# Kernel optimization log

Measured on AMD Instinct MI355X. Metric: run time of the kernel, lower is better.

Reference implementation:

```python
import jax, jax.numpy as jnp
import numpy as np


def setup_inputs() -> dict:
    key = jax.random.key(0)
    kq, kk, kv, km = jax.random.split(key, 4)
    B, H, S, D = 8, 16, 1024, 64
    Q = jax.random.normal(kq, (B, H, S, D), dtype=jnp.float32)
    K = jax.random.normal(kk, (B, H, S, D), dtype=jnp.float32)
    V = jax.random.normal(kv, (B, H, S, D), dtype=jnp.float32)
    # True means masked, per torch masked_fill_ semantics
    attn_mask = jax.random.randint(km, (B, 1, S, S), 0, 2).astype(bool)
    return {"Q": Q, "K": K, "V": V, "attn_mask": attn_mask}


def reference(Q, K, V, attn_mask):
    # Attention(Q,K,V) = softmax(QK^T / sqrt(d_k)) V, with masked scores
    # set to 1e-9 (faithful to the original's masked_fill_(mask, 1e-09)).
    d_k = Q.shape[-1]
    scores = jnp.einsum('bhqd,bhkd->bhqk', Q, K) / jnp.sqrt(jnp.float32(d_k))
    scores = jnp.where(attn_mask, jnp.asarray(1e-9, scores.dtype), scores)
    attn = jax.nn.softmax(scores, axis=-1)          # [B,H,S,S]
    context = jnp.einsum('bhqk,bhkd->bhqd', attn, V)  # [B,H,S,D]
    return (context, attn)
```

## Files before the change

kernel.cpp:

```cpp
#include <hip/hip_runtime.h>
#include <hip/hip_bf16.h>

typedef __attribute__((ext_vector_type(4))) float f32x4;
typedef __attribute__((ext_vector_type(8))) short bf16x8;
typedef __attribute__((ext_vector_type(4))) int   i32x4;
typedef __attribute__((ext_vector_type(4))) unsigned u32x4;

#define S_LEN 1024
#define DQ    64
#define QTL   16
#define VSTR  266
#define PSTR  264
#define CSTR  68
#define PT_BYTES (QTL * PSTR * 2)
#define VT_BYTES (DQ * VSTR * 2)

__device__ __forceinline__ unsigned pk2(float a, float b) {
    union { __hip_bfloat162 h; unsigned u; } v;
    v.h = __float22bfloat162_rn(make_float2(a, b));
    return v.u;
}

__device__ __forceinline__ bf16x8 pack8(float4 a, float4 b) {
    union { bf16x8 v; unsigned u[4]; } r;
    r.u[0] = pk2(a.x, a.y); r.u[1] = pk2(a.z, a.w);
    r.u[2] = pk2(b.x, b.y); r.u[3] = pk2(b.z, b.w);
    return r.v;
}

__device__ __forceinline__ bf16x8 ld_frag2(const unsigned short* p) {
    union { bf16x8 v; unsigned u[4]; } r;
    r.u[0] = *(const unsigned*)(p);
    r.u[1] = *(const unsigned*)(p + 2);
    r.u[2] = *(const unsigned*)(p + 16);
    r.u[3] = *(const unsigned*)(p + 18);
    return r.v;
}

__device__ __forceinline__ float bflo(unsigned u) { union { unsigned x; float f; } v; v.x = u << 16;         return v.f; }
__device__ __forceinline__ float bfhi(unsigned u) { union { unsigned x; float f; } v; v.x = u & 0xffff0000u; return v.f; }

__global__ __launch_bounds__(256) void pack_mask(const int* __restrict__ Mg,
                                                 unsigned long long* __restrict__ Pk) {
    const int gw   = (int)((blockIdx.x * 256 + threadIdx.x) >> 6);
    const int lane = threadIdx.x & 63;
#pragma unroll 4
    for (int j = 0; j < 32; ++j) {
        const size_t g = ((size_t)gw * 32 + j) * 64 + lane;
        const int m = __builtin_nontemporal_load(Mg + g);
        const unsigned long long bal = __ballot(m != 0);
        if (lane == 0) Pk[(size_t)gw * 32 + j] = bal;
    }
}

template <int PACKED>
__global__ __launch_bounds__(512, 6) void attn_fused(
    const float* __restrict__ Qg, const float* __restrict__ Kg,
    const float* __restrict__ Vg, const int* __restrict__ Mg,
    const unsigned* __restrict__ Mb,
    float* __restrict__ Og, float* __restrict__ Ag)
{
    const int tid  = threadIdx.x;
    const int lane = tid & 63;
    const int wc   = tid >> 6;
    const int l15  = lane & 15;
    const int lg   = lane >> 4;

    const int raw  = blockIdx.x;
    const int xcd  = raw & 7;
    const int slot = raw >> 3;
    const int bh   = xcd * 16 + (slot >> 6);
    const int qt   = slot & 63;
    const int b    = bh >> 4;

    const size_t kvbase = (size_t)bh * (S_LEN * DQ);
    const float* Qp = Qg + kvbase + (size_t)qt * (QTL * DQ);
    const float* Kp = Kg + kvbase;
    const float* Vp = Vg + kvbase;
    float*       Ap = Ag + (size_t)bh * (size_t)(S_LEN * S_LEN) + (size_t)(qt * QTL) * S_LEN;
    float*       Op = Og + kvbase + (size_t)qt * (QTL * DQ);

    __shared__ __align__(16) unsigned char smem[PT_BYTES + VT_BYTES];
    unsigned short* Pt  = (unsigned short*)smem;
    float*          red = (float*)smem;
    float*          Cx  = (float*)smem;
    unsigned short* Vt  = (unsigned short*)(smem + PT_BYTES);
    float*          Tt  = (float*)(smem + PT_BYTES);

    const int qrow = l15;

    unsigned mwd[4];
    if (PACKED) {
        const unsigned* mw = Mb + ((size_t)b * S_LEN + qt * QTL + qrow) * 32 + wc;
#pragma unroll
        for (int i = 0; i < 4; ++i) mwd[i] = mw[i * 8];
    }

    bf16x8 aq0, aq1;
    {
        const float* qr = Qp + (size_t)qrow * DQ + lg * 4;
        aq0 = pack8(*(const float4*)(qr),      *(const float4*)(qr + 16));
        aq1 = pack8(*(const float4*)(qr + 32), *(const float4*)(qr + 48));
    }

    f32x4 sc[8];
#pragma unroll
    for (int t = 0; t < 8; ++t) sc[t] = (f32x4){0.f, 0.f, 0.f, 0.f};

#pragma unroll
    for (int i = 0; i < 4; ++i)
#pragma unroll
        for (int h = 0; h < 2; ++h) {
            const float* krow = Kp + (size_t)(i * 256 + wc * 32 + h * 16 + l15) * DQ + lg * 4;
            const bf16x8 k0 = pack8(*(const float4*)(krow),      *(const float4*)(krow + 16));
            const bf16x8 k1 = pack8(*(const float4*)(krow + 32), *(const float4*)(krow + 48));
            f32x4 acc = sc[i * 2 + h];
            acc = __builtin_amdgcn_mfma_f32_16x16x32_bf16(k0, aq0, acc, 0, 0, 0);
            acc = __builtin_amdgcn_mfma_f32_16x16x32_bf16(k1, aq1, acc, 0, 0, 0);
            sc[i * 2 + h] = acc;
        }

    if (PACKED) {
#pragma unroll
        for (int i = 0; i < 4; ++i)
#pragma unroll
            for (int h = 0; h < 2; ++h) {
                const int t = i * 2 + h;
#pragma unroll
                for (int r = 0; r < 4; ++r)
                    sc[t][r] = ((mwd[i] >> (h * 16 + lg * 4 + r)) & 1u) ? 1e-9f
                                                                        : sc[t][r] * 0.125f;
            }
    } else {
        const int* mrow = Mg + (size_t)b * (size_t)(S_LEN * S_LEN)
                        + (size_t)(qt * QTL + qrow) * S_LEN + wc * 32 + lg * 4;
#pragma unroll
        for (int i = 0; i < 4; ++i)
#pragma unroll
            for (int h = 0; h < 2; ++h) {
                const i32x4 m4 = *(const i32x4*)(mrow + i * 256 + h * 16);
                const int t = i * 2 + h;
#pragma unroll
                for (int r = 0; r < 4; ++r)
                    sc[t][r] = m4[r] ? 1e-9f : sc[t][r] * 0.125f;
            }
    }

#pragma unroll
    for (int g = 0; g < 2; ++g) {
        float4 vv[4];
#pragma unroll
        for (int j = 0; j < 4; ++j)
            vv[j] = *(const float4*)(Vp + (size_t)((g * 4 + j) * 512 + tid) * 4);
#pragma unroll
        for (int j = 0; j < 4; ++j) {
            const int f = ((g * 4 + j) * 512 + tid) * 4;
            const int k = f >> 6, d = f & 63;
            const unsigned u0 = pk2(vv[j].x, vv[j].y);
            const unsigned u1 = pk2(vv[j].z, vv[j].w);
            Vt[(d + 0) * VSTR + k] = (unsigned short)u0;
            Vt[(d + 1) * VSTR + k] = (unsigned short)(u0 >> 16);
            Vt[(d + 2) * VSTR + k] = (unsigned short)u1;
            Vt[(d + 3) * VSTR + k] = (unsigned short)(u1 >> 16);
        }
    }

    float rsum = 0.f;
#pragma unroll
    for (int t = 0; t < 8; ++t)
#pragma unroll
        for (int r = 0; r < 4; ++r) {
            const float p = __expf(sc[t][r]);
            sc[t][r] = p;
            rsum += p;
        }
    rsum += __shfl_xor(rsum, 16);
    rsum += __shfl_xor(rsum, 32);
    __syncthreads();
    if (lane < 16) red[qrow * 8 + wc] = rsum;
    __syncthreads();
    float rinv;
    {
        const f32x4 a = *(const f32x4*)(red + qrow * 8);
        const f32x4 bq = *(const f32x4*)(red + qrow * 8 + 4);
        rinv = 1.0f / ((a[0] + a[1] + a[2] + a[3]) + (bq[0] + bq[1] + bq[2] + bq[3]));
    }
#pragma unroll
    for (int t = 0; t < 8; ++t)
#pragma unroll
        for (int r = 0; r < 4; ++r) sc[t][r] *= rinv;

    bf16x8 paf[4];
#pragma unroll
    for (int i = 0; i < 4; ++i) {
        union { bf16x8 v; unsigned u[4]; } pa;
        pa.u[0] = pk2(sc[i * 2][0],     sc[i * 2][1]);
        pa.u[1] = pk2(sc[i * 2][2],     sc[i * 2][3]);
        pa.u[2] = pk2(sc[i * 2 + 1][0], sc[i * 2 + 1][1]);
        pa.u[3] = pk2(sc[i * 2 + 1][2], sc[i * 2 + 1][3]);
        paf[i] = pa.v;
    }
    __syncthreads();

    f32x4 co[4];
#pragma unroll
    for (int m = 0; m < 4; ++m) co[m] = (f32x4){0.f, 0.f, 0.f, 0.f};

#pragma unroll
    for (int i = 0; i < 4; ++i) {
        if (i > 0) {
#pragma unroll
            for (int g = 0; g < 2; ++g) {
                float4 vv[4];
#pragma unroll
                for (int j = 0; j < 4; ++j)
                    vv[j] = *(const float4*)(Vp + (size_t)i * (256 * DQ)
                                             + (size_t)((g * 4 + j) * 512 + tid) * 4);
#pragma unroll
                for (int j = 0; j < 4; ++j) {
                    const int f = ((g * 4 + j) * 512 + tid) * 4;
                    const int k = f >> 6, d = f & 63;
                    const unsigned u0 = pk2(vv[j].x, vv[j].y);
                    const unsigned u1 = pk2(vv[j].z, vv[j].w);
                    Vt[(d + 0) * VSTR + k] = (unsigned short)u0;
                    Vt[(d + 1) * VSTR + k] = (unsigned short)(u0 >> 16);
                    Vt[(d + 2) * VSTR + k] = (unsigned short)u1;
                    Vt[(d + 3) * VSTR + k] = (unsigned short)(u1 >> 16);
                }
            }
        }

        {
            union { bf16x8 v; unsigned long long q[2]; } pa;
            pa.v = paf[i];
            unsigned short* prow = Pt + qrow * PSTR + wc * 32 + lg * 4;
            *(unsigned long long*)(prow)      = pa.q[0];
            *(unsigned long long*)(prow + 16) = pa.q[1];
        }
        __syncthreads();

        {
            const int row = tid >> 5, c8 = tid & 31;
            const u32x4 u = *(const u32x4*)(Pt + row * PSTR + c8 * 8);
            const f32x4 o0 = { bflo(u[0]), bfhi(u[0]), bflo(u[1]), bfhi(u[1]) };
            const f32x4 o1 = { bflo(u[2]), bfhi(u[2]), bflo(u[3]), bfhi(u[3]) };
            float* dst = Ap + (size_t)row * S_LEN + i * 256 + c8 * 8;
            __builtin_nontemporal_store(o0, (f32x4*)(dst));
            __builtin_nontemporal_store(o1, (f32x4*)(dst + 4));
        }

#pragma unroll
        for (int m = 0; m < 4; ++m) {
            const bf16x8 bv = ld_frag2(Vt + (size_t)(m * 16 + l15) * VSTR + wc * 32 + lg * 4);
            co[m] = __builtin_amdgcn_mfma_f32_16x16x32_bf16(paf[i], bv, co[m], 0, 0, 0);
        }
        __syncthreads();
    }

    if (wc > 0) {
        float* T = Tt + (size_t)(wc - 1) * (QTL * CSTR);
#pragma unroll
        for (int m = 0; m < 4; ++m)
#pragma unroll
            for (int r = 0; r < 4; ++r)
                T[(lg * 4 + r) * CSTR + m * 16 + l15] = co[m][r];
    }
    __syncthreads();
    if (wc == 0) {
#pragma unroll
        for (int m = 0; m < 4; ++m)
#pragma unroll
            for (int r = 0; r < 4; ++r) {
                float acc = co[m][r];
#pragma unroll
                for (int s = 0; s < 7; ++s)
                    acc += Tt[(size_t)s * (QTL * CSTR) + (lg * 4 + r) * CSTR + m * 16 + l15];
                Cx[(lg * 4 + r) * CSTR + m * 16 + l15] = acc;
            }
    }
    __syncthreads();

    if (tid < 256) {
        const int row = tid >> 4, col = (tid & 15) * 4;
        const f32x4 o = *(const f32x4*)(Cx + (size_t)row * CSTR + col);
        __builtin_nontemporal_store(o, (f32x4*)(Op + (size_t)row * DQ + col));
    }
}

extern "C" void kernel_launch(void* const* d_in, const int* in_sizes, int n_in,
                              void* d_out, int out_size, void* d_ws, size_t ws_size,
                              hipStream_t stream) {
    const float* Q = (const float*)d_in[0];
    const float* K = (const float*)d_in[1];
    const float* V = (const float*)d_in[2];
    const int*   M = (const int*)d_in[3];
    float* ctx  = (float*)d_out;
    float* attn = ctx + (size_t)8 * 16 * 1024 * 64;

    const size_t packed_bytes = (size_t)8 * 1024 * 1024 / 8;
    if (ws_size >= packed_bytes) {
        pack_mask<<<dim3(1024), dim3(256), 0, stream>>>(M, (unsigned long long*)d_ws);
        attn_fused<1><<<dim3(8192), dim3(512), 0, stream>>>(
            Q, K, V, M, (const unsigned*)d_ws, ctx, attn);
    } else {
        attn_fused<0><<<dim3(8192), dim3(512), 0, stream>>>(
            Q, K, V, M, nullptr, ctx, attn);
    }
}
```

Baseline: 413.6 us.

## Split fused attention into separate score/softmax and PV kernels

Splits the single fused kernel into one kernel that computes masked scores, softmax, and writes the fp32 attention matrix, and a second kernel that reads that matrix back with V to compute the context. This frees registers and shared memory in each kernel and allows higher occupancy. In exchange, the full attention matrix must be re-read from memory. The stored probabilities are now full fp32 instead of bf16-rounded.

```diff
diff --git a/kernel.cpp b/kernel.cpp
--- a/kernel.cpp
+++ b/kernel.cpp
@@ -4,16 +4,14 @@
 typedef __attribute__((ext_vector_type(4))) float f32x4;
 typedef __attribute__((ext_vector_type(8))) short bf16x8;
 typedef __attribute__((ext_vector_type(4))) int   i32x4;
-typedef __attribute__((ext_vector_type(4))) unsigned u32x4;
 
 #define S_LEN 1024
 #define DQ    64
 #define QTL   16
 #define VSTR  266
-#define PSTR  264
 #define CSTR  68
-#define PT_BYTES (QTL * PSTR * 2)
-#define VT_BYTES (DQ * VSTR * 2)
+#define VT_SH (DQ * VSTR)
+#define RED_FLOATS (8 * QTL * CSTR)
 
 __device__ __forceinline__ unsigned pk2(float a, float b) {
     union { __hip_bfloat162 h; unsigned u; } v;
@@ -36,9 +34,6 @@
     r.u[3] = *(const unsigned*)(p + 18);
     return r.v;
 }
-
-__device__ __forceinline__ float bflo(unsigned u) { union { unsigned x; float f; } v; v.x = u << 16;         return v.f; }
-__device__ __forceinline__ float bfhi(unsigned u) { union { unsigned x; float f; } v; v.x = u & 0xffff0000u; return v.f; }
 
 __global__ __launch_bounds__(256) void pack_mask(const int* __restrict__ Mg,
                                                  unsigned long long* __restrict__ Pk) {
@@ -54,11 +49,10 @@
 }
 
 template <int PACKED>
-__global__ __launch_bounds__(512, 6) void attn_fused(
+__global__ __launch_bounds__(512, 8) void attn_score(
     const float* __restrict__ Qg, const float* __restrict__ Kg,
-    const float* __restrict__ Vg, const int* __restrict__ Mg,
-    const unsigned* __restrict__ Mb,
-    float* __restrict__ Og, float* __restrict__ Ag)
+    const int* __restrict__ Mg, const unsigned* __restrict__ Mb,
+    float* __restrict__ Ag)
 {
     const int tid  = threadIdx.x;
     const int lane = tid & 63;
@@ -76,25 +70,10 @@
     const size_t kvbase = (size_t)bh * (S_LEN * DQ);
     const float* Qp = Qg + kvbase + (size_t)qt * (QTL * DQ);
     const float* Kp = Kg + kvbase;
-    const float* Vp = Vg + kvbase;
     float*       Ap = Ag + (size_t)bh * (size_t)(S_LEN * S_LEN) + (size_t)(qt * QTL) * S_LEN;
-    float*       Op = Og + kvbase + (size_t)qt * (QTL * DQ);
-
-    __shared__ __align__(16) unsigned char smem[PT_BYTES + VT_BYTES];
-    unsigned short* Pt  = (unsigned short*)smem;
-    float*          red = (float*)smem;
-    float*          Cx  = (float*)smem;
-    unsigned short* Vt  = (unsigned short*)(smem + PT_BYTES);
-    float*          Tt  = (float*)(smem + PT_BYTES);
-
+
+    __shared__ float red[QTL * 8];
     const int qrow = l15;
-
-    unsigned mwd[4];
-    if (PACKED) {
-        const unsigned* mw = Mb + ((size_t)b * S_LEN + qt * QTL + qrow) * 32 + wc;
-#pragma unroll
-        for (int i = 0; i < 4; ++i) mwd[i] = mw[i * 8];
-    }
 
     bf16x8 aq0, aq1;
     {
@@ -121,16 +100,19 @@
         }
 
     if (PACKED) {
-#pragma unroll
-        for (int i = 0; i < 4; ++i)
+        const unsigned* mw = Mb + ((size_t)b * S_LEN + qt * QTL + qrow) * 32 + wc;
+#pragma unroll
+        for (int i = 0; i < 4; ++i) {
+            const unsigned w = mw[i * 8];
 #pragma unroll
             for (int h = 0; h < 2; ++h) {
                 const int t = i * 2 + h;
 #pragma unroll
                 for (int r = 0; r < 4; ++r)
-                    sc[t][r] = ((mwd[i] >> (h * 16 + lg * 4 + r)) & 1u) ? 1e-9f
-                                                                        : sc[t][r] * 0.125f;
-            }
+                    sc[t][r] = ((w >> (h * 16 + lg * 4 + r)) & 1u) ? 1e-9f
+                                                                   : sc[t][r] * 0.125f;
+            }
+        }
     } else {
         const int* mrow = Mg + (size_t)b * (size_t)(S_LEN * S_LEN)
                         + (size_t)(qt * QTL + qrow) * S_LEN + wc * 32 + lg * 4;
@@ -144,25 +126,6 @@
                 for (int r = 0; r < 4; ++r)
                     sc[t][r] = m4[r] ? 1e-9f : sc[t][r] * 0.125f;
             }
-    }
-
-#pragma unroll
-    for (int g = 0; g < 2; ++g) {
-        float4 vv[4];
-#pragma unroll
-        for (int j = 0; j < 4; ++j)
-            vv[j] = *(const float4*)(Vp + (size_t)((g * 4 + j) * 512 + tid) * 4);
-#pragma unroll
-        for (int j = 0; j < 4; ++j) {
-            const int f = ((g * 4 + j) * 512 + tid) * 4;
-            const int k = f >> 6, d = f & 63;
-            const unsigned u0 = pk2(vv[j].x, vv[j].y);
-            const unsigned u1 = pk2(vv[j].z, vv[j].w);
-            Vt[(d + 0) * VSTR + k] = (unsigned short)u0;
-            Vt[(d + 1) * VSTR + k] = (unsigned short)(u0 >> 16);
-            Vt[(d + 2) * VSTR + k] = (unsigned short)u1;
-            Vt[(d + 3) * VSTR + k] = (unsigned short)(u1 >> 16);
-        }
     }
 
     float rsum = 0.f;
@@ -176,7 +139,6 @@
         }
     rsum += __shfl_xor(rsum, 16);
     rsum += __shfl_xor(rsum, 32);
-    __syncthreads();
     if (lane < 16) red[qrow * 8 + wc] = rsum;
     __syncthreads();
     float rinv;
@@ -185,74 +147,86 @@
         const f32x4 bq = *(const f32x4*)(red + qrow * 8 + 4);
         rinv = 1.0f / ((a[0] + a[1] + a[2] + a[3]) + (bq[0] + bq[1] + bq[2] + bq[3]));
     }
-#pragma unroll
-    for (int t = 0; t < 8; ++t)
-#pragma unroll
-        for (int r = 0; r < 4; ++r) sc[t][r] *= rinv;
-
-    bf16x8 paf[4];
+
+    float* arow = Ap + (size_t)qrow * S_LEN + wc * 32 + lg * 4;
 #pragma unroll
     for (int i = 0; i < 4; ++i) {
+        f32x4 o0 = sc[i * 2 + 0], o1 = sc[i * 2 + 1];
+#pragma unroll
+        for (int r = 0; r < 4; ++r) { o0[r] *= rinv; o1[r] *= rinv; }
+        __builtin_nontemporal_store(o0, (f32x4*)(arow + i * 256));
+        __builtin_nontemporal_store(o1, (f32x4*)(arow + i * 256 + 16));
+    }
+}
+
+__global__ __launch_bounds__(512, 8) void attn_pv(
+    const float* __restrict__ Vg, const float* __restrict__ Ag,
+    float* __restrict__ Og)
+{
+    const int tid  = threadIdx.x;
+    const int lane = tid & 63;
+    const int wc   = tid >> 6;
+    const int l15  = lane & 15;
+    const int lg   = lane >> 4;
+
+    const int raw  = blockIdx.x;
+    const int xcd  = raw & 7;
+    const int slot = raw >> 3;
+    const int bh   = xcd * 16 + (slot >> 6);
+    const int qt   = slot & 63;
+
+    const size_t kvbase = (size_t)bh * (S_LEN * DQ);
+    const float* Vp = Vg + kvbase;
+    const float* Ap = Ag + (size_t)bh * (size_t)(S_LEN * S_LEN) + (size_t)(qt * QTL) * S_LEN;
+    float*       Op = Og + kvbase + (size_t)qt * (QTL * DQ);
+
+    __shared__ __align__(16) unsigned char smem[RED_FLOATS * 4];
+    unsigned short* Vt = (unsigned short*)smem;
+    float*          Tt = (float*)smem;
+    float*          Cx = (float*)smem + 7 * (QTL * CSTR);
+
+    const int qrow = l15;
+
+    f32x4 co[4];
+#pragma unroll
+    for (int m = 0; m < 4; ++m) co[m] = (f32x4){0.f, 0.f, 0.f, 0.f};
+
+#pragma unroll
+    for (int i = 0; i < 4; ++i) {
+#pragma unroll
+        for (int g = 0; g < 2; ++g) {
+            float4 vv[4];
+#pragma unroll
+            for (int j = 0; j < 4; ++j)
+                vv[j] = *(const float4*)(Vp + (size_t)i * (256 * DQ)
+                                         + (size_t)((g * 4 + j) * 512 + tid) * 4);
+#pragma unroll
+            for (int j = 0; j < 4; ++j) {
+                const int f = ((g * 4 + j) * 512 + tid) * 4;
+                const int k = f >> 6, d = f & 63;
+                const unsigned u0 = pk2(vv[j].x, vv[j].y);
+                const unsigned u1 = pk2(vv[j].z, vv[j].w);
+                Vt[(d + 0) * VSTR + k] = (unsigned short)u0;
+                Vt[(d + 1) * VSTR + k] = (unsigned short)(u0 >> 16);
+                Vt[(d + 2) * VSTR + k] = (unsigned short)u1;
+                Vt[(d + 3) * VSTR + k] = (unsigned short)(u1 >> 16);
+            }
+        }
+
+        const float* arow = Ap + (size_t)qrow * S_LEN + i * 256 + wc * 32 + lg * 4;
+        const f32x4 p0 = *(const f32x4*)(arow);
+        const f32x4 p1 = *(const f32x4*)(arow + 16);
         union { bf16x8 v; unsigned u[4]; } pa;
-        pa.u[0] = pk2(sc[i * 2][0],     sc[i * 2][1]);
-        pa.u[1] = pk2(sc[i * 2][2],     sc[i * 2][3]);
-        pa.u[2] = pk2(sc[i * 2 + 1][0], sc[i * 2 + 1][1]);
-        pa.u[3] = pk2(sc[i * 2 + 1][2], sc[i * 2 + 1][3]);
-        paf[i] = pa.v;
-    }
-    __syncthreads();
-
-    f32x4 co[4];
-#pragma unroll
-    for (int m = 0; m < 4; ++m) co[m] = (f32x4){0.f, 0.f, 0.f, 0.f};
-
-#pragma unroll
-    for (int i = 0; i < 4; ++i) {
-        if (i > 0) {
-#pragma unroll
-            for (int g = 0; g < 2; ++g) {
-                float4 vv[4];
-#pragma unroll
-                for (int j = 0; j < 4; ++j)
-                    vv[j] = *(const float4*)(Vp + (size_t)i * (256 * DQ)
-                                             + (size_t)((g * 4 + j) * 512 + tid) * 4);
-#pragma unroll
-                for (int j = 0; j < 4; ++j) {
-                    const int f = ((g * 4 + j) * 512 + tid) * 4;
-                    const int k = f >> 6, d = f & 63;
-                    const unsigned u0 = pk2(vv[j].x, vv[j].y);
-                    const unsigned u1 = pk2(vv[j].z, vv[j].w);
-                    Vt[(d + 0) * VSTR + k] = (unsigned short)u0;
-                    Vt[(d + 1) * VSTR + k] = (unsigned short)(u0 >> 16);
-                    Vt[(d + 2) * VSTR + k] = (unsigned short)u1;
-                    Vt[(d + 3) * VSTR + k] = (unsigned short)(u1 >> 16);
-                }
-            }
-        }
-
-        {
-            union { bf16x8 v; unsigned long long q[2]; } pa;
-            pa.v = paf[i];
-            unsigned short* prow = Pt + qrow * PSTR + wc * 32 + lg * 4;
-            *(unsigned long long*)(prow)      = pa.q[0];
-            *(unsigned long long*)(prow + 16) = pa.q[1];
-        }
+        pa.u[0] = pk2(p0[0], p0[1]);
+        pa.u[1] = pk2(p0[2], p0[3]);
+        pa.u[2] = pk2(p1[0], p1[1]);
+        pa.u[3] = pk2(p1[2], p1[3]);
+
         __syncthreads();
-
-        {
-            const int row = tid >> 5, c8 = tid & 31;
-            const u32x4 u = *(const u32x4*)(Pt + row * PSTR + c8 * 8);
-            const f32x4 o0 = { bflo(u[0]), bfhi(u[0]), bflo(u[1]), bfhi(u[1]) };
-            const f32x4 o1 = { bflo(u[2]), bfhi(u[2]), bflo(u[3]), bfhi(u[3]) };
-            float* dst = Ap + (size_t)row * S_LEN + i * 256 + c8 * 8;
-            __builtin_nontemporal_store(o0, (f32x4*)(dst));
-            __builtin_nontemporal_store(o1, (f32x4*)(dst + 4));
-        }
-
 #pragma unroll
         for (int m = 0; m < 4; ++m) {
             const bf16x8 bv = ld_frag2(Vt + (size_t)(m * 16 + l15) * VSTR + wc * 32 + lg * 4);
-            co[m] = __builtin_amdgcn_mfma_f32_16x16x32_bf16(paf[i], bv, co[m], 0, 0, 0);
+            co[m] = __builtin_amdgcn_mfma_f32_16x16x32_bf16(pa.v, bv, co[m], 0, 0, 0);
         }
         __syncthreads();
     }
@@ -300,10 +274,11 @@
     const size_t packed_bytes = (size_t)8 * 1024 * 1024 / 8;
     if (ws_size >= packed_bytes) {
         pack_mask<<<dim3(1024), dim3(256), 0, stream>>>(M, (unsigned long long*)d_ws);
-        attn_fused<1><<<dim3(8192), dim3(512), 0, stream>>>(
-            Q, K, V, M, (const unsigned*)d_ws, ctx, attn);
+        attn_score<1><<<dim3(8192), dim3(512), 0, stream>>>(
+            Q, K, M, (const unsigned*)d_ws, attn);
     } else {
-        attn_fused<0><<<dim3(8192), dim3(512), 0, stream>>>(
-            Q, K, V, M, nullptr, ctx, attn);
-    }
-}
+        attn_score<0><<<dim3(8192), dim3(512), 0, stream>>>(
+            Q, K, M, nullptr, attn);
+    }
+    attn_pv<<<dim3(8192), dim3(512), 0, stream>>>(V, attn, ctx);
+}
```

After: 580.0 us. 40.2% more time.
